# Performance work log

Measured on AMD Instinct MI355X. Metric: run time of the kernel, lower is better.

The kernel has to match this reference:

```python
import jax, jax.numpy as jnp
import numpy as np

DIM = 2048
NUM_EXPERTS = 64
K = 2


def setup_inputs() -> dict:
    key = jax.random.key(0)
    kx, kw, kb = jax.random.split(key, 3)
    x = jax.random.normal(kx, (4, 8192, DIM), dtype=jnp.float32)
    # nn.Linear(dim, num_experts): weight [E, dim], bias [E]
    bound = 1.0 / np.sqrt(DIM)
    W = jax.random.uniform(kw, (NUM_EXPERTS, DIM), minval=-bound, maxval=bound, dtype=jnp.float32)
    b = jax.random.uniform(kb, (NUM_EXPERTS,), minval=-bound, maxval=bound, dtype=jnp.float32)
    return {"x": x, "W": W, "b": b}


def reference(x, W, b):
    # gate_logits = x @ W.T + b  -> [B, S, E]
    gate_logits = jnp.einsum("bsd,ed->bse", x, W) + b
    gate_scores = jax.nn.softmax(gate_logits, axis=-1)
    topk_scores, topk_idx = jax.lax.top_k(gate_scores, K)  # [B, S, K]
    return gate_scores, topk_idx, topk_scores
```

## Files before the change

### kernel.cpp

```cpp
#include <hip/hip_runtime.h>
#include <hip/hip_bf16.h>
#include <stdint.h>
#include <stddef.h>

#define DIM   2048
#define NEXP  64
#define NTOK  32768
#define KF    64
#define OFF_IDX  (NTOK*NEXP)
#define OFF_TSC  (OFF_IDX + NTOK*2)
#define TAU   5e-4f

typedef __attribute__((ext_vector_type(8))) short  short8;
typedef __attribute__((ext_vector_type(4))) float  f32x4;

__device__ __forceinline__ unsigned short bf16_rne(float f) {
    unsigned u = __builtin_bit_cast(unsigned, f);
    u += 0x7fffu + ((u >> 16) & 1u);
    return (unsigned short)(u >> 16);
}
__device__ __forceinline__ float bf16_up(unsigned short s) {
    unsigned u = ((unsigned)s) << 16;
    return __builtin_bit_cast(float, u);
}

__global__ __launch_bounds__(256) void wsplit(const float* __restrict__ W,
                                              short* __restrict__ warr,
                                              int* __restrict__ cnt) {
    int idx  = blockIdx.x * 256 + threadIdx.x;
    if (idx == 0) *cnt = 0;
    int j    = idx & 7;
    int lane = (idx >> 3) & 63;
    int nf   = (idx >> 9) & 3;
    int kf   = (idx >> 11) & 63;
    int term = idx >> 17;
    int e = nf * 16 + (lane & 15);
    int d = kf * 32 + (lane >> 4) * 8 + j;
    float w = W[e * DIM + d];
    unsigned short h  = bf16_rne(w);
    float r1 = w - bf16_up(h);
    unsigned short md = bf16_rne(r1);
    warr[idx] = (short)((term == 0) ? h : md);
}

__device__ __forceinline__ bool gtie(float a, int ia, float b, int ib) {
    return (a > b) || (a == b && ia < ib);
}

__global__ __launch_bounds__(512, 4) void router_mfma(
        const float* __restrict__ X, const short* __restrict__ Wsp,
        const float* __restrict__ bias, float* __restrict__ out,
        int* __restrict__ cnt, int* __restrict__ list) {
    __shared__ char smem[65536] __attribute__((aligned(16)));
    const int tid  = threadIdx.x;
    const int lane = tid & 63;
    const int w    = tid >> 6;
    const int wq   = w & 3;
    const int kh   = w >> 2;
    const int tok0 = blockIdx.x * 64 + wq * 16;
    const int l15  = lane & 15;
    const int l4   = lane >> 4;

    const int q2  = tid >> 7;
    const int khs = q2 >> 1, ts = q2 & 1;
    const int li  = tid & 127;
    const char* wsrc = (const char*)Wsp + ((size_t)ts * 64 + khs * 32) * 4096 + li * 16;
    char* bdst = smem + q2 * 16384 + li * 16;

    const float* xr = X + (size_t)(tok0 + l15) * DIM + kh * 1024 + l4 * 8;
    const char*  bq = smem + (kh * 2) * 16384 + lane * 16;

    f32x4 acc[4];
#pragma unroll
    for (int n = 0; n < 4; n++) acc[n] = (f32x4)0.0f;

    f32x4 a_pf[4][2];
#pragma unroll
    for (int p = 0; p < 4; p++) {
        a_pf[p][0] = *(const f32x4*)(xr + p * 32);
        a_pf[p][1] = *(const f32x4*)(xr + p * 32 + 4);
    }

#pragma unroll 1
    for (int g = 0; g < 8; ++g) {
        __syncthreads();
        {
            const char* s0 = wsrc + g * 16384;
            f32x4 ld[8];
#pragma unroll
            for (int i = 0; i < 8; i++) ld[i] = *(const f32x4*)(s0 + i * 2048);
#pragma unroll
            for (int i = 0; i < 8; i++) *(f32x4*)(bdst + i * 2048) = ld[i];
        }
        __syncthreads();

#pragma unroll
        for (int p = 0; p < 4; ++p) {
            const int lkf = g * 4 + p;
            const int kn  = (lkf + 4 < 32) ? lkf + 4 : 31;

            f32x4 a0 = a_pf[p][0], a1 = a_pf[p][1];
            a_pf[p][0] = *(const f32x4*)(xr + kn * 32);
            a_pf[p][1] = *(const f32x4*)(xr + kn * 32 + 4);

            short8 b[2][4];
#pragma unroll
            for (int t = 0; t < 2; t++)
#pragma unroll
                for (int n = 0; n < 4; n++)
                    b[t][n] = *(const short8*)(bq + t * 16384 + p * 4096 + n * 1024);

            short8 ah, am;
#pragma unroll
            for (int j = 0; j < 8; j++) {
                float v = (j < 4) ? a0[j & 3] : a1[j & 3];
                unsigned short h  = bf16_rne(v);
                float r1 = v - bf16_up(h);
                unsigned short md = bf16_rne(r1);
                ah[j] = (short)h;
                am[j] = (short)md;
            }

#pragma unroll
            for (int n = 0; n < 4; n++) {
                f32x4 c = acc[n];
                c = __builtin_amdgcn_mfma_f32_16x16x32_bf16(ah, b[0][n], c, 0, 0, 0);
                c = __builtin_amdgcn_mfma_f32_16x16x32_bf16(ah, b[1][n], c, 0, 0, 0);
                c = __builtin_amdgcn_mfma_f32_16x16x32_bf16(am, b[0][n], c, 0, 0, 0);
                c = __builtin_amdgcn_mfma_f32_16x16x32_bf16(am, b[1][n], c, 0, 0, 0);
                acc[n] = c;
            }
        }
    }

    __syncthreads();
    if (kh == 1) {
#pragma unroll
        for (int n = 0; n < 4; n++)
            *(f32x4*)(smem + ((size_t)(wq * 4 + n)) * 1024 + lane * 16) = acc[n];
    }
    __syncthreads();
    if (kh == 1) return;
#pragma unroll
    for (int n = 0; n < 4; n++)
        acc[n] += *(const f32x4*)(smem + ((size_t)(wq * 4 + n)) * 1024 + lane * 16);

    float bv[4];
#pragma unroll
    for (int n = 0; n < 4; n++) bv[n] = bias[n * 16 + l15];

#pragma unroll
    for (int r = 0; r < 4; r++) {
        const int t = tok0 + l4 * 4 + r;
        float v[4];
#pragma unroll
        for (int n = 0; n < 4; n++) v[n] = acc[n][r] + bv[n];

        float mx = fmaxf(fmaxf(v[0], v[1]), fmaxf(v[2], v[3]));
#pragma unroll
        for (int s = 1; s < 16; s <<= 1) mx = fmaxf(mx, __shfl_xor(mx, s, 64));

        float p[4], den = 0.0f;
#pragma unroll
        for (int n = 0; n < 4; n++) { p[n] = __expf(v[n] - mx); den += p[n]; }
#pragma unroll
        for (int s = 1; s < 16; s <<= 1) den += __shfl_xor(den, s, 64);
        const float inv = 1.0f / den;
#pragma unroll
        for (int n = 0; n < 4; n++)
            out[(size_t)t * 64 + n * 16 + l15] = p[n] * inv;

        float v1 = -3.4e38f, v2 = -3.4e38f, v3 = -3.4e38f;
        int   i1 = 9999,     i2 = 9999,     i3 = 9999;
#pragma unroll
        for (int n = 0; n < 4; n++) {
            float vv = v[n]; int ii = n * 16 + l15;
            if (gtie(vv, ii, v1, i1))      { v3=v2;i3=i2; v2=v1;i2=i1; v1=vv;i1=ii; }
            else if (gtie(vv, ii, v2, i2)) { v3=v2;i3=i2; v2=vv;i2=ii; }
            else if (gtie(vv, ii, v3, i3)) { v3=vv;i3=ii; }
        }
#pragma unroll
        for (int s = 1; s < 16; s <<= 1) {
            float ov1=__shfl_xor(v1,s,64), ov2=__shfl_xor(v2,s,64), ov3=__shfl_xor(v3,s,64);
            int   oi1=__shfl_xor(i1,s,64), oi2=__shfl_xor(i2,s,64), oi3=__shfl_xor(i3,s,64);
            bool a1 = gtie(v1,i1,ov1,oi1);
            float w1 = a1?v1:ov1;  int k1 = a1?i1:oi1;
            float x1 = a1?v2:ov2;  int xi1= a1?i2:oi2;
            float x2 = a1?v3:ov3;  int xi2= a1?i3:oi3;
            float y1 = a1?ov1:v1;  int yi1= a1?oi1:i1;
            float y2 = a1?ov2:v2;  int yi2= a1?oi2:i2;
            bool a2 = gtie(x1,xi1,y1,yi1);
            float w2 = a2?x1:y1;   int k2 = a2?xi1:yi1;
            float w3; int k3;
            if (a2) { bool a3 = gtie(x2,xi2,y1,yi1); w3 = a3?x2:y1; k3 = a3?xi2:yi1; }
            else    { bool a3 = gtie(x1,xi1,y2,yi2); w3 = a3?x1:y2; k3 = a3?xi1:yi2; }
            v1=w1;i1=k1; v2=w2;i2=k2; v3=w3;i3=k3;
        }
        if (l15 == 0) {
            out[OFF_IDX + (size_t)t * 2 + 0] = (float)i1;
            out[OFF_IDX + (size_t)t * 2 + 1] = (float)i2;
            out[OFF_TSC + (size_t)t * 2 + 0] = __expf(v1 - mx) * inv;
            out[OFF_TSC + (size_t)t * 2 + 1] = __expf(v2 - mx) * inv;
            if ((v1 - v2 < TAU) || (v2 - v3 < TAU)) {
                int slot = atomicAdd(cnt, 1);
                list[slot] = t;
            }
        }
    }
}

__global__ __launch_bounds__(256, 2) void router_exact(
        const float* __restrict__ X, const float* __restrict__ W,
        const float* __restrict__ Bb, float* __restrict__ out,
        const int* __restrict__ cnt, const int* __restrict__ list) {
    __shared__ float xrow[2048];
    __shared__ char  wbuf[2][64 * 272] __attribute__((aligned(16)));
    const int tid = threadIdx.x;
    const int n   = *cnt;

    for (int ii = blockIdx.x; ii < n; ii += gridDim.x) {
        const int t = list[ii];
#pragma unroll
        for (int q = 0; q < 2; ++q) {
            int s = tid + q * 256;
            *(f32x4*)&xrow[s * 4] = *(const f32x4*)(X + (size_t)t * DIM + s * 4);
        }
#pragma unroll
        for (int q = 0; q < 4; ++q) {
            int s = tid + q * 256;
            int e = s >> 4, dq = s & 15;
            f32x4 wv = *(const f32x4*)(W + (size_t)e * DIM + dq * 4);
            *(f32x4*)(wbuf[0] + e * 272 + ((16 * dq) ^ ((e & 7) << 4))) = wv;
        }
        __syncthreads();

        float acc = 0.0f;
#pragma unroll 1
        for (int c = 0; c < 32; ++c) {
            if (c + 1 < 32) {
#pragma unroll
                for (int q = 0; q < 4; ++q) {
                    int s = tid + q * 256;
                    int e = s >> 4, dq = s & 15;
                    f32x4 wv = *(const f32x4*)(W + (size_t)e * DIM + (c + 1) * 64 + dq * 4);
                    *(f32x4*)(wbuf[(c + 1) & 1] + e * 272 + ((16 * dq) ^ ((e & 7) << 4))) = wv;
                }
            }
            if (tid < 64) {
                const char* wb = wbuf[c & 1] + tid * 272;
                const int sw = (tid & 7) << 4;
#pragma unroll
                for (int dq = 0; dq < 16; ++dq) {
                    f32x4 xq = *(const f32x4*)&xrow[c * 64 + dq * 4];
                    f32x4 wv = *(const f32x4*)(wb + ((16 * dq) ^ sw));
#pragma unroll
                    for (int j = 0; j < 4; ++j)
                        acc = fmaf(xq[j], wv[j], acc);
                }
            }
            __syncthreads();
        }

        if (tid < 64) {
            const int lane = tid;
            const float lg = acc + Bb[lane];
            float m = lg;
#pragma unroll
            for (int s = 1; s < 64; s <<= 1) m = fmaxf(m, __shfl_xor(m, s, 64));
            const float p = __expf(lg - m);
            float den = p;
#pragma unroll
            for (int s = 1; s < 64; s <<= 1) den += __shfl_xor(den, s, 64);
            const float inv = 1.0f / den;
            out[(size_t)t * 64 + lane] = p * inv;

            float v1 = lg, v2 = -3.4e38f;
            int   i1 = lane, i2 = 127;
#pragma unroll
            for (int s = 1; s < 64; s <<= 1) {
                float ov1 = __shfl_xor(v1, s, 64), ov2 = __shfl_xor(v2, s, 64);
                int   oi1 = __shfl_xor(i1, s, 64), oi2 = __shfl_xor(i2, s, 64);
                bool  aw  = gtie(v1, i1, ov1, oi1);
                float nv1 = aw ? v1 : ov1;  int ni1 = aw ? i1 : oi1;
                float cv  = aw ? ov1 : v1;  int ci  = aw ? oi1 : i1;
                float sv  = aw ? v2 : ov2;  int si  = aw ? i2 : oi2;
                bool  c2  = gtie(cv, ci, sv, si);
                v1 = nv1; i1 = ni1;
                v2 = c2 ? cv : sv; i2 = c2 ? ci : si;
            }
            if (lane == 0) {
                out[OFF_IDX + (size_t)t * 2 + 0] = (float)i1;
                out[OFF_IDX + (size_t)t * 2 + 1] = (float)i2;
                out[OFF_TSC + (size_t)t * 2 + 0] = __expf(v1 - m) * inv;
                out[OFF_TSC + (size_t)t * 2 + 1] = __expf(v2 - m) * inv;
            }
        }
        __syncthreads();
    }
}

extern "C" void kernel_launch(void* const* d_in, const int* in_sizes, int n_in,
                              void* d_out, int out_size, void* d_ws, size_t ws_size,
                              hipStream_t stream) {
    const float* X = (const float*)d_in[0];
    const float* W = (const float*)d_in[1];
    const float* b = (const float*)d_in[2];
    float* out  = (float*)d_out;
    short* Wsp  = (short*)d_ws;
    int*   cnt  = (int*)((char*)d_ws + 524288);
    int*   list = (int*)((char*)d_ws + 524292);

    wsplit<<<1024, 256, 0, stream>>>(W, Wsp, cnt);
    router_mfma<<<NTOK / 64, 512, 0, stream>>>(X, Wsp, b, out, cnt, list);
    router_exact<<<512, 256, 0, stream>>>(X, W, b, out, cnt, list);
}
```

Baseline: 105.7 us.

## Double-buffer weight tiles in LDS with register prefetch across k-steps

Replaces the load-sync-compute loop over 8 large weight chunks with a 16-step loop that uses two 32KB LDS buffers. Each step issues the global loads for the next weight chunk into registers before the MFMA work, then writes them to the other buffer afterwards, so only one barrier is needed per step. The aim is to hide global weight-load latency behind compute. The X prefetch distance shrinks from 4 to 2 k-blocks, and the sched_barrier constrains how the compiler can schedule around the loads.

```diff
diff --git a/kernel.cpp b/kernel.cpp
--- a/kernel.cpp
+++ b/kernel.cpp
@@ -61,43 +61,59 @@
     const int l15  = lane & 15;
     const int l4   = lane >> 4;
 
-    const int q2  = tid >> 7;
-    const int khs = q2 >> 1, ts = q2 & 1;
-    const int li  = tid & 127;
-    const char* wsrc = (const char*)Wsp + ((size_t)ts * 64 + khs * 32) * 4096 + li * 16;
-    char* bdst = smem + q2 * 16384 + li * 16;
+    const char* wbytes = (const char*)Wsp;
 
     const float* xr = X + (size_t)(tok0 + l15) * DIM + kh * 1024 + l4 * 8;
-    const char*  bq = smem + (kh * 2) * 16384 + lane * 16;
 
     f32x4 acc[4];
 #pragma unroll
     for (int n = 0; n < 4; n++) acc[n] = (f32x4)0.0f;
 
-    f32x4 a_pf[4][2];
-#pragma unroll
-    for (int p = 0; p < 4; p++) {
+    f32x4 a_pf[2][2];
+#pragma unroll
+    for (int p = 0; p < 2; p++) {
         a_pf[p][0] = *(const f32x4*)(xr + p * 32);
         a_pf[p][1] = *(const f32x4*)(xr + p * 32 + 4);
     }
 
+    {
+        f32x4 bst[4];
+#pragma unroll
+        for (int j = 0; j < 4; j++) {
+            const int u   = tid * 64 + j * 16;
+            const int pi  = u >> 12;
+            const int inn = u & 4095;
+            const int term = pi >> 2, kh2 = (pi >> 1) & 1, p = pi & 1;
+            bst[j] = *(const f32x4*)(wbytes + ((size_t)(term * 64 + kh2 * 32 + p)) * 4096 + inn);
+        }
+#pragma unroll
+        for (int j = 0; j < 4; j++)
+            *(f32x4*)(smem + tid * 64 + j * 16) = bst[j];
+    }
+    __syncthreads();
+
 #pragma unroll 1
-    for (int g = 0; g < 8; ++g) {
-        __syncthreads();
-        {
-            const char* s0 = wsrc + g * 16384;
-            f32x4 ld[8];
-#pragma unroll
-            for (int i = 0; i < 8; i++) ld[i] = *(const f32x4*)(s0 + i * 2048);
-#pragma unroll
-            for (int i = 0; i < 8; i++) *(f32x4*)(bdst + i * 2048) = ld[i];
-        }
-        __syncthreads();
-
-#pragma unroll
-        for (int p = 0; p < 4; ++p) {
-            const int lkf = g * 4 + p;
-            const int kn  = (lkf + 4 < 32) ? lkf + 4 : 31;
+    for (int g = 0; g < 16; ++g) {
+        const int cur = (g & 1) * 32768;
+
+        f32x4 bst[4];
+        if (g < 15) {
+#pragma unroll
+            for (int j = 0; j < 4; j++) {
+                const int u   = tid * 64 + j * 16;
+                const int pi  = u >> 12;
+                const int inn = u & 4095;
+                const int term = pi >> 2, kh2 = (pi >> 1) & 1, p = pi & 1;
+                bst[j] = *(const f32x4*)(wbytes
+                          + ((size_t)(term * 64 + kh2 * 32 + (g + 1) * 2 + p)) * 4096 + inn);
+            }
+            __builtin_amdgcn_sched_barrier(0);
+        }
+
+#pragma unroll
+        for (int p = 0; p < 2; ++p) {
+            const int lkf = g * 2 + p;
+            const int kn  = (lkf + 2 < 32) ? lkf + 2 : 31;
 
             f32x4 a0 = a_pf[p][0], a1 = a_pf[p][1];
             a_pf[p][0] = *(const f32x4*)(xr + kn * 32);
@@ -108,7 +124,8 @@
             for (int t = 0; t < 2; t++)
 #pragma unroll
                 for (int n = 0; n < 4; n++)
-                    b[t][n] = *(const short8*)(bq + t * 16384 + p * 4096 + n * 1024);
+                    b[t][n] = *(const short8*)(smem + cur + ((t * 2 + kh) * 2 + p) * 4096
+                                               + n * 1024 + lane * 16);
 
             short8 ah, am;
 #pragma unroll
@@ -131,9 +148,16 @@
                 acc[n] = c;
             }
         }
-    }
-
-    __syncthreads();
+
+        if (g < 15) {
+            char* nb = smem + ((g + 1) & 1) * 32768;
+#pragma unroll
+            for (int j = 0; j < 4; j++)
+                *(f32x4*)(nb + tid * 64 + j * 16) = bst[j];
+        }
+        __syncthreads();
+    }
+
     if (kh == 1) {
 #pragma unroll
         for (int n = 0; n < 4; n++)
```

Result: no change. 104.8 us (-0.9%).
